# Kernel optimization log

Hardware: AMD Instinct MI355X
Metric: run time of the kernel (lower is better)

## Reference

```python
import jax, jax.numpy as jnp
import numpy as np

N_NODES = 100000


def gcn_conv(x, src, dst, norm, W, b, n):
    # x: [N, F_in]; src/dst: [E'] (with self loops); norm: [E']
    xw = x @ W                                   # [N, F_out]
    msg = xw[src] * norm[:, None]                # [E', F_out]
    agg = jax.ops.segment_sum(msg, dst, num_segments=n)
    return agg + b


def _self_loops_and_norm(edge_index, n):
    loop = jnp.arange(n, dtype=edge_index.dtype)
    src = jnp.concatenate([edge_index[0], loop])
    dst = jnp.concatenate([edge_index[1], loop])
    deg = jax.ops.segment_sum(jnp.ones_like(dst, dtype=jnp.float32), dst, num_segments=n)
    dis = jnp.where(deg > 0, jax.lax.rsqrt(jnp.maximum(deg, 1.0)), 0.0)
    norm = dis[src] * dis[dst]
    return src, dst, norm


def setup_inputs() -> dict:
    key = jax.random.key(0)
    k1, k2, k3, k4, k5, k6 = jax.random.split(key, 6)
    n, e = N_NODES, 1600000
    f_in, f_hid, f_out = 64, 128, 64
    x = jax.random.normal(k1, (n, f_in), dtype=jnp.float32)
    edge_index = jax.random.randint(k2, (2, e), 0, n, dtype=jnp.int64)
    # Glorot init like PyG GCNConv
    W0 = jax.random.normal(k3, (f_in, f_hid), dtype=jnp.float32) * (1.0 / np.sqrt(f_in))
    b0 = jnp.zeros((f_hid,), dtype=jnp.float32)
    W1 = jax.random.normal(k4, (f_hid, f_out), dtype=jnp.float32) * (1.0 / np.sqrt(f_hid))
    b1 = jnp.zeros((f_out,), dtype=jnp.float32)
    return {"x": x, "edge_index": edge_index, "W0": W0, "b0": b0, "W1": W1, "b1": b1}


def reference(x, edge_index, W0, b0, W1, b1):
    n = x.shape[0]
    src, dst, norm = _self_loops_and_norm(edge_index, n)
    h = gcn_conv(x, src, dst, norm, W0, b0, n)
    h = jax.nn.relu(h)
    out = gcn_conv(h, src, dst, norm, W1, b1, n)
    return jax.nn.sigmoid(out)
```

## Files before the change

### kernel.cpp

```cpp
#include <hip/hip_runtime.h>
#include <hip/hip_fp16.h>
#include <math.h>


#define FIN 64
#define FHID 128
#define FOUT 64
#define NPB 128
#define LOGNPB 7
#define BMAX 800
#define G 128


__global__ __launch_bounds__(256) void khist(const int* __restrict__ dst,
                                             int* __restrict__ ghist,
                                             int e, int B, int chunk) {
    __shared__ int h[BMAX];
    int g = blockIdx.x, t = threadIdx.x;
    for (int i = t; i < B; i += 256) h[i] = 0;
    __syncthreads();
    int lo = g * chunk, hi = min(e, lo + chunk);
    for (int i = lo + t; i < hi; i += 256)
        atomicAdd(&h[dst[i] >> LOGNPB], 1);
    __syncthreads();
    for (int i = t; i < B; i += 256) ghist[i * G + g] = h[i];
}

__global__ __launch_bounds__(256) void kscanA(const int* __restrict__ ghist,
                                              int* __restrict__ gbase,
                                              int* __restrict__ tot, int B) {
    int per = (B + gridDim.x - 1) / gridDim.x;
    int b0 = blockIdx.x * per, b1 = min(B, b0 + per);
    for (int b = b0 + threadIdx.x; b < b1; b += 256) {
        int run = 0;
        #pragma unroll 8
        for (int g = 0; g < G; ++g) {
            int v = ghist[b * G + g];
            gbase[b * G + g] = run;
            run += v;
        }
        tot[b] = run;
    }
}

__global__ __launch_bounds__(256) void kscanB(const int* __restrict__ tot,
                                              int* __restrict__ bb, int B, int e) {
    __shared__ int s[256];
    __shared__ int chunkoff;
    int t = threadIdx.x;
    if (t == 0) chunkoff = 0;
    __syncthreads();
    for (int c0 = 0; c0 < B; c0 += 256) {
        int v = (c0 + t < B) ? tot[c0 + t] : 0;
        s[t] = v;
        __syncthreads();
        for (int off = 1; off < 256; off <<= 1) {
            int u = (t >= off) ? s[t - off] : 0;
            __syncthreads();
            s[t] += u;
            __syncthreads();
        }
        if (c0 + t < B) bb[c0 + t] = s[t] - v + chunkoff;
        __syncthreads();
        if (t == 255) chunkoff += s[255];
        __syncthreads();
    }
    if (t == 0) bb[B] = e;
}

__global__ __launch_bounds__(256) void kscatter(const int* __restrict__ src,
                                                const int* __restrict__ dst,
                                                const int* __restrict__ gbase,
                                                const int* __restrict__ bb,
                                                unsigned* __restrict__ pk,
                                                int e, int B, int chunk) {
    __shared__ int cur[BMAX];
    int g = blockIdx.x, t = threadIdx.x;
    for (int b = t; b < B; b += 256) cur[b] = bb[b] + gbase[b * G + g];
    __syncthreads();
    int lo = g * chunk, hi = min(e, lo + chunk);
    for (int i = lo + t; i < hi; i += 256) {
        int d = dst[i], s = src[i], b = d >> LOGNPB;
        int p = atomicAdd(&cur[b], 1);
        pk[p] = ((unsigned)(d & (NPB - 1)) << 17) | (unsigned)s;
    }
}

__global__ __launch_bounds__(256) void kpsort(const unsigned* __restrict__ pk,
                                              const int* __restrict__ bb,
                                              int* __restrict__ ssrc,
                                              int* __restrict__ rp,
                                              float* __restrict__ dis,
                                              int n, int e) {
    __shared__ int cnt[NPB];
    __shared__ int pre[NPB];
    int b = blockIdx.x, t = threadIdx.x;
    if (t < NPB) cnt[t] = 0;
    __syncthreads();
    int lo = bb[b], hi = bb[b + 1];
    for (int i = lo + t; i < hi; i += 256)
        atomicAdd(&cnt[pk[i] >> 17], 1);
    __syncthreads();
    if (t < NPB) pre[t] = cnt[t];
    __syncthreads();
    #pragma unroll
    for (int off = 1; off < NPB; off <<= 1) {
        int v = (t < NPB && t >= off) ? pre[t - off] : 0;
        __syncthreads();
        if (t < NPB) pre[t] += v;
        __syncthreads();
    }
    if (t < NPB) {
        int node = b * NPB + t;
        int bs = lo + pre[t] - cnt[t];
        if (node < n) {
            rp[node] = bs;
            dis[node] = rsqrtf(1.0f + (float)cnt[t]);
        }
        cnt[t] = bs;
    }
    if (b == 0 && t == 0) rp[n] = e;
    __syncthreads();
    for (int i = lo + t; i < hi; i += 256) {
        unsigned v = pk[i];
        int p = atomicAdd(&cnt[v >> 17], 1);
        ssrc[p] = (int)(v & 0x1FFFF);
    }
}

__global__ void k_toy(const float* __restrict__ x, const float* __restrict__ dis,
                      __half* __restrict__ yh, int n) {
    int gid = blockIdx.x * blockDim.x + threadIdx.x;
    if (gid >= n * 16) return;
    int node = gid >> 4;
    float d = dis[node];
    float4 v = reinterpret_cast<const float4*>(x)[gid];
    __half2 h0, h1;
    h0.x = __float2half(d * v.x); h0.y = __float2half(d * v.y);
    h1.x = __float2half(d * v.z); h1.y = __float2half(d * v.w);
    reinterpret_cast<__half2*>(yh)[gid * 2 + 0] = h0;
    reinterpret_cast<__half2*>(yh)[gid * 2 + 1] = h1;
}

__global__ __launch_bounds__(256) void k_pull16(
        const int* __restrict__ rp, const int* __restrict__ ssrc,
        const float* __restrict__ dis, const __half* __restrict__ yh,
        const float* __restrict__ b1, float* __restrict__ outp,
        int n, int sig) {
    int node4 = blockIdx.x * 4 + (threadIdx.x >> 6);
    if (node4 >= n) return;
    int node = __builtin_amdgcn_readfirstlane(node4);
    int f = threadIdx.x & 63;
    float acc0 = __half2float(yh[(size_t)node * 64 + f]);
    float acc1 = 0.0f, acc2 = 0.0f, acc3 = 0.0f;
    int j = rp[node], end = rp[node + 1];
    for (; j + 3 < end; j += 4) {
        int s0 = ssrc[j], s1 = ssrc[j + 1], s2 = ssrc[j + 2], s3 = ssrc[j + 3];
        acc0 += __half2float(yh[(size_t)s0 * 64 + f]);
        acc1 += __half2float(yh[(size_t)s1 * 64 + f]);
        acc2 += __half2float(yh[(size_t)s2 * 64 + f]);
        acc3 += __half2float(yh[(size_t)s3 * 64 + f]);
    }
    for (; j < end; ++j)
        acc0 += __half2float(yh[(size_t)ssrc[j] * 64 + f]);
    float v = dis[node] * ((acc0 + acc1) + (acc2 + acc3));
    if (sig) {
        v += b1[f];
        v = 1.0f / (1.0f + expf(-v));
    }
    outp[(size_t)node * 64 + f] = v;
}

__global__ __launch_bounds__(256) void k_gemm1(
        const float* __restrict__ in,
        const float* __restrict__ W0,
        const float* __restrict__ b0,
        __half* __restrict__ h,
        int n, int nwaves) {
    int gw = blockIdx.x * 4 + (threadIdx.x >> 6);
    int lane = threadIdx.x & 63;
    int half_ = gw & 1;
    int col = half_ * 64 + lane;

    float w0r[64];
    #pragma unroll
    for (int k = 0; k < 64; ++k) w0r[k] = W0[k * FHID + col];
    float bias = b0[col];

    for (int task = gw; task < 2 * n; task += nwaves) {
        int row = __builtin_amdgcn_readfirstlane(task >> 1);
        const float* srow = in + (size_t)row * FIN;
        float acc = bias;
        #pragma unroll
        for (int k = 0; k < 64; ++k) acc = fmaf(srow[k], w0r[k], acc);
        h[(size_t)row * FHID + col] = __float2half(fmaxf(acc, 0.0f));
    }
}

__global__ __launch_bounds__(256) void k_gemm2(
        const __half* __restrict__ h,
        const float* __restrict__ W1,
        const float* __restrict__ dis,
        __half* __restrict__ yh,
        int n, int nwaves) {
    int gw = blockIdx.x * 4 + (threadIdx.x >> 6);
    int lane = threadIdx.x & 63;

    float w1r[128];
    #pragma unroll
    for (int k = 0; k < 128; ++k) w1r[k] = W1[k * FOUT + lane];

    for (int task = gw; task < n; task += nwaves) {
        int row = __builtin_amdgcn_readfirstlane(task);
        const __half2* hrow = reinterpret_cast<const __half2*>(
            h + (size_t)row * FHID);
        float acc = 0.0f;
        #pragma unroll
        for (int k = 0; k < 64; ++k) {
            __half2 hv = hrow[k];
            acc = fmaf(__half2float(hv.x), w1r[2 * k + 0], acc);
            acc = fmaf(__half2float(hv.y), w1r[2 * k + 1], acc);
        }
        yh[(size_t)row * FOUT + lane] = __float2half(dis[row] * acc);
    }
}

extern "C" void kernel_launch(void* const* d_in, const int* in_sizes, int n_in,
                              void* d_out, int out_size, void* d_ws, size_t ws_size,
                              hipStream_t stream) {
    const float* x   = (const float*)d_in[0];
    const int*   ei  = (const int*)d_in[1];
    const float* W0  = (const float*)d_in[2];
    const float* b0  = (const float*)d_in[3];
    const float* W1  = (const float*)d_in[4];
    const float* b1  = (const float*)d_in[5];
    float*       out = (float*)d_out;

    const int n = in_sizes[0] / FIN;
    const int e = in_sizes[1] / 2;
    const int* src = ei;
    const int* dst = ei + e;
    if (n > (1 << 17)) return;

    const int B = (n + NPB - 1) / NPB;
    if (B > BMAX) return;
    const int chunk = (e + G - 1) / G;

    float*    dis  = (float*)d_ws;
    float*    buf  = dis + n;
    int*      ssrc = (int*)(buf + (size_t)n * FIN);
    int*      rp   = ssrc + e;
    __half*   yh   = (__half*)(rp + (n + 1));
    char*     region = (char*)(yh + (size_t)n * FIN);
    __half*   hh   = (__half*)region;
    unsigned* pk   = (unsigned*)region;
    int*      ghist = (int*)(pk + e);
    int*      gbase = ghist + (size_t)B * G;
    int*      tot   = gbase + (size_t)B * G;
    int*      bb    = tot + B;
    size_t region_sz = (size_t)n * FHID * sizeof(__half);
    {
        size_t pkchain = (size_t)((char*)(bb + B + 1) - region);
        if (pkchain > region_sz) region_sz = pkchain;
    }
    size_t need = (size_t)(region - (char*)d_ws) + region_sz;
    if (ws_size < need) return;

    khist<<<G, 256, 0, stream>>>(dst, ghist, e, B, chunk);
    kscanA<<<8, 256, 0, stream>>>(ghist, gbase, tot, B);
    kscanB<<<1, 256, 0, stream>>>(tot, bb, B, e);
    kscatter<<<G, 256, 0, stream>>>(src, dst, gbase, bb, pk, e, B, chunk);
    kpsort<<<B, 256, 0, stream>>>(pk, bb, ssrc, rp, dis, n, e);

    k_toy<<<(n * 16 + 255) / 256, 256, 0, stream>>>(x, dis, yh, n);
    k_pull16<<<(n + 3) / 4, 256, 0, stream>>>(rp, ssrc, dis, yh, b1, buf, n, 0);

    const int blocks = 2048, nwaves = blocks * 4;
    k_gemm1<<<blocks, 256, 0, stream>>>(buf, W0, b0, hh, n, nwaves);
    k_gemm2<<<blocks, 256, 0, stream>>>(hh, W1, dis, yh, n, nwaves);

    k_pull16<<<(n + 3) / 4, 256, 0, stream>>>(rp, ssrc, dis, yh, b1, out, n, 1);
}
```

Before: 271.5 us.

## Fuse x scaling into per-bucket sort, stage sorted indices in LDS, unroll gather by 8

```diff
diff --git a/kernel.cpp b/kernel.cpp
--- a/kernel.cpp
+++ b/kernel.cpp
@@ -10,6 +10,7 @@
 #define LOGNPB 7
 #define BMAX 800
 #define G 128
+#define CAP 4096
 
 
 __global__ __launch_bounds__(256) void khist(const int* __restrict__ dst,
@@ -88,16 +89,20 @@
 
 __global__ __launch_bounds__(256) void kpsort(const unsigned* __restrict__ pk,
                                               const int* __restrict__ bb,
+                                              const float* __restrict__ x,
                                               int* __restrict__ ssrc,
                                               int* __restrict__ rp,
                                               float* __restrict__ dis,
+                                              __half* __restrict__ yh,
                                               int n, int e) {
     __shared__ int cnt[NPB];
     __shared__ int pre[NPB];
+    __shared__ float disl[NPB];
+    __shared__ unsigned stage[CAP];
     int b = blockIdx.x, t = threadIdx.x;
+    int lo = bb[b], hi = bb[b + 1], m = hi - lo;
     if (t < NPB) cnt[t] = 0;
     __syncthreads();
-    int lo = bb[b], hi = bb[b + 1];
     for (int i = lo + t; i < hi; i += 256)
         atomicAdd(&cnt[pk[i] >> 17], 1);
     __syncthreads();
@@ -112,34 +117,46 @@
     }
     if (t < NPB) {
         int node = b * NPB + t;
-        int bs = lo + pre[t] - cnt[t];
+        int c = cnt[t];
+        int bs = lo + pre[t] - c;
+        float dv = rsqrtf(1.0f + (float)c);
+        disl[t] = dv;
         if (node < n) {
             rp[node] = bs;
-            dis[node] = rsqrtf(1.0f + (float)cnt[t]);
-        }
-        cnt[t] = bs;
+            dis[node] = dv;
+        }
+        cnt[t] = bs - lo;
     }
     if (b == 0 && t == 0) rp[n] = e;
     __syncthreads();
-    for (int i = lo + t; i < hi; i += 256) {
-        unsigned v = pk[i];
-        int p = atomicAdd(&cnt[v >> 17], 1);
-        ssrc[p] = (int)(v & 0x1FFFF);
-    }
-}
-
-__global__ void k_toy(const float* __restrict__ x, const float* __restrict__ dis,
-                      __half* __restrict__ yh, int n) {
-    int gid = blockIdx.x * blockDim.x + threadIdx.x;
-    if (gid >= n * 16) return;
-    int node = gid >> 4;
-    float d = dis[node];
-    float4 v = reinterpret_cast<const float4*>(x)[gid];
-    __half2 h0, h1;
-    h0.x = __float2half(d * v.x); h0.y = __float2half(d * v.y);
-    h1.x = __float2half(d * v.z); h1.y = __float2half(d * v.w);
-    reinterpret_cast<__half2*>(yh)[gid * 2 + 0] = h0;
-    reinterpret_cast<__half2*>(yh)[gid * 2 + 1] = h1;
+    if (m <= CAP) {
+        for (int i = lo + t; i < hi; i += 256) {
+            unsigned v = pk[i];
+            int p = atomicAdd(&cnt[v >> 17], 1);
+            stage[p] = v & 0x1FFFF;
+        }
+        __syncthreads();
+        for (int i = t; i < m; i += 256) ssrc[lo + i] = (int)stage[i];
+    } else {
+        for (int i = lo + t; i < hi; i += 256) {
+            unsigned v = pk[i];
+            int p = atomicAdd(&cnt[v >> 17], 1);
+            ssrc[lo + p] = (int)(v & 0x1FFFF);
+        }
+    }
+    for (int i = t; i < NPB * 16; i += 256) {
+        int node = b * NPB + (i >> 4);
+        if (node < n) {
+            float d = disl[i >> 4];
+            int gi = b * (NPB * 16) + i;
+            float4 v = reinterpret_cast<const float4*>(x)[gi];
+            __half2 h0, h1;
+            h0.x = __float2half(d * v.x); h0.y = __float2half(d * v.y);
+            h1.x = __float2half(d * v.z); h1.y = __float2half(d * v.w);
+            reinterpret_cast<__half2*>(yh)[gi * 2 + 0] = h0;
+            reinterpret_cast<__half2*>(yh)[gi * 2 + 1] = h1;
+        }
+    }
 }
 
 __global__ __launch_bounds__(256) void k_pull16(
@@ -151,19 +168,29 @@
     if (node4 >= n) return;
     int node = __builtin_amdgcn_readfirstlane(node4);
     int f = threadIdx.x & 63;
-    float acc0 = __half2float(yh[(size_t)node * 64 + f]);
-    float acc1 = 0.0f, acc2 = 0.0f, acc3 = 0.0f;
+    float a0 = __half2float(yh[(size_t)node * 64 + f]);
+    float a1 = 0.f, a2 = 0.f, a3 = 0.f, a4 = 0.f, a5 = 0.f, a6 = 0.f, a7 = 0.f;
     int j = rp[node], end = rp[node + 1];
-    for (; j + 3 < end; j += 4) {
-        int s0 = ssrc[j], s1 = ssrc[j + 1], s2 = ssrc[j + 2], s3 = ssrc[j + 3];
-        acc0 += __half2float(yh[(size_t)s0 * 64 + f]);
-        acc1 += __half2float(yh[(size_t)s1 * 64 + f]);
-        acc2 += __half2float(yh[(size_t)s2 * 64 + f]);
-        acc3 += __half2float(yh[(size_t)s3 * 64 + f]);
-    }
-    for (; j < end; ++j)
-        acc0 += __half2float(yh[(size_t)ssrc[j] * 64 + f]);
-    float v = dis[node] * ((acc0 + acc1) + (acc2 + acc3));
+    for (; j + 7 < end; j += 8) {
+        int s0 = ssrc[j],     s1 = ssrc[j + 1], s2 = ssrc[j + 2], s3 = ssrc[j + 3];
+        int s4 = ssrc[j + 4], s5 = ssrc[j + 5], s6 = ssrc[j + 6], s7 = ssrc[j + 7];
+        a0 += __half2float(yh[(size_t)s0 * 64 + f]);
+        a1 += __half2float(yh[(size_t)s1 * 64 + f]);
+        a2 += __half2float(yh[(size_t)s2 * 64 + f]);
+        a3 += __half2float(yh[(size_t)s3 * 64 + f]);
+        a4 += __half2float(yh[(size_t)s4 * 64 + f]);
+        a5 += __half2float(yh[(size_t)s5 * 64 + f]);
+        a6 += __half2float(yh[(size_t)s6 * 64 + f]);
+        a7 += __half2float(yh[(size_t)s7 * 64 + f]);
+    }
+    for (; j + 1 < end; j += 2) {
+        int s0 = ssrc[j], s1 = ssrc[j + 1];
+        a0 += __half2float(yh[(size_t)s0 * 64 + f]);
+        a1 += __half2float(yh[(size_t)s1 * 64 + f]);
+    }
+    if (j < end)
+        a0 += __half2float(yh[(size_t)ssrc[j] * 64 + f]);
+    float v = dis[node] * (((a0 + a1) + (a2 + a3)) + ((a4 + a5) + (a6 + a7)));
     if (sig) {
         v += b1[f];
         v = 1.0f / (1.0f + expf(-v));
@@ -270,9 +297,8 @@
     kscanA<<<8, 256, 0, stream>>>(ghist, gbase, tot, B);
     kscanB<<<1, 256, 0, stream>>>(tot, bb, B, e);
     kscatter<<<G, 256, 0, stream>>>(src, dst, gbase, bb, pk, e, B, chunk);
-    kpsort<<<B, 256, 0, stream>>>(pk, bb, ssrc, rp, dis, n, e);
-
-    k_toy<<<(n * 16 + 255) / 256, 256, 0, stream>>>(x, dis, yh, n);
+    kpsort<<<B, 256, 0, stream>>>(pk, bb, x, ssrc, rp, dis, yh, n, e);
+
     k_pull16<<<(n + 3) / 4, 256, 0, stream>>>(rp, ssrc, dis, yh, b1, buf, n, 0);
 
     const int blocks = 2048, nwaves = blocks * 4;
```

New measurement: 259.5 us. -4.4%, faster.
